# Kernel optimization log

Measured on AMD Instinct MI355X. Metric: run time of the kernel, lower is better.

The kernel has to match this reference:

```python
import jax, jax.numpy as jnp
import numpy as np

B, DX, DY, H, K = 16384, 128, 128, 2048, 16
MIN_BIN = 1e-3   # min bin width/height (nflows convention)
MIN_DERIV = 1e-3  # min knot derivative


def setup_inputs() -> dict:
    key = jax.random.key(0)
    k0, k1, k2, k3 = jax.random.split(key, 4)
    x = jax.random.normal(k0, (B, DX), jnp.float32)
    y = jax.random.uniform(k1, (B, DY), jnp.float32, minval=1e-4, maxval=1.0 - 1e-4)
    W1 = jax.random.normal(k2, (DX, H), jnp.float32) / np.sqrt(DX).astype(np.float32)
    b1 = jnp.zeros((H,), jnp.float32)
    W2 = jax.random.normal(k3, (H, DY * (3 * K + 1)), jnp.float32) / np.sqrt(H).astype(np.float32)
    b2 = jnp.zeros((DY * (3 * K + 1),), jnp.float32)
    return {"x": x, "y": y, "W1": W1, "b1": b1, "W2": W2, "b2": b2}


def _rq_spline(y, pdf):
    # y: [B, D] in (0,1); pdf: [B, D, 3K+1] unnormalized spline params
    w_un, h_un, d_un = pdf[..., :K], pdf[..., K:2 * K], pdf[..., 2 * K:]
    widths = MIN_BIN + (1.0 - K * MIN_BIN) * jax.nn.softmax(w_un, axis=-1)   # [B,D,K]
    heights = MIN_BIN + (1.0 - K * MIN_BIN) * jax.nn.softmax(h_un, axis=-1)  # [B,D,K]
    derivs = MIN_DERIV + jax.nn.softplus(d_un)                               # [B,D,K+1]

    pad = [(0, 0), (0, 0), (1, 0)]
    cw = jnp.pad(jnp.cumsum(widths, axis=-1), pad)    # knot x-positions [B,D,K+1]
    ch = jnp.pad(jnp.cumsum(heights, axis=-1), pad)   # knot y-positions [B,D,K+1]

    # data-dependent bin lookup (searchsorted equivalent, vectorized)
    idx = jnp.clip(jnp.sum(y[..., None] >= cw, axis=-1) - 1, 0, K - 1)  # [B,D]
    g = lambda a: jnp.take_along_axis(a, idx[..., None], axis=-1)[..., 0]
    xk, yk = g(cw), g(ch)
    wk, hk = g(widths), g(heights)
    dk = g(derivs)
    dk1 = jnp.take_along_axis(derivs, idx[..., None] + 1, axis=-1)[..., 0]

    s = hk / wk                      # bin slope
    t = (y - xk) / wk                # theta in [0,1]
    omt = 1.0 - t
    denom = s + (dk1 + dk - 2.0 * s) * t * omt
    out = yk + hk * (s * t * t + dk * t * omt) / denom
    deriv = s * s * (dk1 * t * t + 2.0 * s * t * omt + dk * omt * omt) / (denom * denom)
    dlogp = jnp.sum(jnp.log(deriv), axis=-1, keepdims=True)  # [B,1]
    return out, dlogp


def reference(x, y, W1, b1, W2, b2):
    # conditioner MLP: x -> spline params
    h = jax.nn.relu(x @ W1 + b1)
    pdf = (h @ W2 + b2).reshape(x.shape[0], DY, 3 * K + 1)
    return _rq_spline(y, pdf)
```

## Files before the change

### kernel.cpp

```cpp
#include <hip/hip_runtime.h>
#include <hip/hip_fp16.h>
#include <cstdint>
#include <cstddef>

#define B_ROWS 16384
#define DX 128
#define DYDIM 128
#define HDIM 2048
#define NPARAM 49
#define NCOL 6272
#define NPAD 6400

typedef __attribute__((ext_vector_type(8))) _Float16 half8v;
typedef __attribute__((ext_vector_type(4))) float f32x4;

__global__ void k_f32_to_f16(const float* __restrict__ in, _Float16* __restrict__ out, int n) {
  int i = blockIdx.x * 256 + threadIdx.x;
  if (i < n) out[i] = (_Float16)in[i];
}

__global__ void k_transpose_f16(const float* __restrict__ in, _Float16* __restrict__ out, int R, int C) {
  __shared__ float tile[32][33];
  int c0 = blockIdx.x * 32, r0 = blockIdx.y * 32;
  int tx = threadIdx.x;
  for (int i = threadIdx.y; i < 32; i += 8)
    tile[i][tx] = in[(size_t)(r0 + i) * C + c0 + tx];
  __syncthreads();
  for (int i = threadIdx.y; i < 32; i += 8)
    out[(size_t)(c0 + i) * R + r0 + tx] = (_Float16)tile[tx][i];
}

__global__ __launch_bounds__(256) void k_gemm1(
    const _Float16* __restrict__ A, const _Float16* __restrict__ Bt,
    const float* __restrict__ bias, _Float16* __restrict__ C,
    int M, int N, int K) {
  __shared__ _Float16 Abuf[128 * 32];
  __shared__ _Float16 Bbuf[128 * 32];
  const int t = threadIdx.x;
  const int l = t & 63;
  const int w = t >> 6;
  int bx = blockIdx.x, by = blockIdx.y;
  {
    const int nx = gridDim.x;
    const int nwg = nx * gridDim.y;
    const int lin = by * nx + bx;
    const int cpx = nwg >> 3;
    const int sw = (lin & 7) * cpx + (lin >> 3);
    bx = sw % nx;
    by = sw / nx;
  }
  const int tileM = by * 128;
  const int tileN = bx * 128;
  const int wm = w >> 1, wn = w & 1;
  const int srow = w * 16 + (l >> 2);
  const int skel = (l & 3) * 8;
  const char* Ag = (const char*)(A + (size_t)(tileM + srow) * K + skel);
  const char* Bg = (const char*)(Bt + (size_t)(tileN + srow) * K + skel);
  const size_t gRowStep = (size_t)64 * K * 2;
  auto ldsA = (__attribute__((address_space(3))) char*)Abuf;
  auto ldsB = (__attribute__((address_space(3))) char*)Bbuf;
  const int ldsBase = w * 1024;
  f32x4 acc[4][4];
#pragma unroll
  for (int i = 0; i < 4; ++i)
#pragma unroll
    for (int j = 0; j < 4; ++j) acc[i][j] = (f32x4){0.f, 0.f, 0.f, 0.f};
  const int nk = K >> 5;
#define STAGE1(kt)                                                                             \
  do {                                                                                         \
    size_t koff = (size_t)(kt) * 64;                                                           \
    __builtin_amdgcn_global_load_lds(                                                          \
        (const __attribute__((address_space(1))) uint32_t*)(Ag + koff),                        \
        (__attribute__((address_space(3))) uint32_t*)(ldsA + ldsBase), 16, 0, 0);              \
    __builtin_amdgcn_global_load_lds(                                                          \
        (const __attribute__((address_space(1))) uint32_t*)(Ag + koff + gRowStep),             \
        (__attribute__((address_space(3))) uint32_t*)(ldsA + 4096 + ldsBase), 16, 0, 0);       \
    __builtin_amdgcn_global_load_lds(                                                          \
        (const __attribute__((address_space(1))) uint32_t*)(Bg + koff),                        \
        (__attribute__((address_space(3))) uint32_t*)(ldsB + ldsBase), 16, 0, 0);              \
    __builtin_amdgcn_global_load_lds(                                                          \
        (const __attribute__((address_space(1))) uint32_t*)(Bg + koff + gRowStep),             \
        (__attribute__((address_space(3))) uint32_t*)(ldsB + 4096 + ldsBase), 16, 0, 0);       \
  } while (0)
  STAGE1(0);
  const int abase = (wm * 64 + (l & 15)) * 32 + (l >> 4) * 8;
  const int bbase = (wn * 64 + (l & 15)) * 32 + (l >> 4) * 8;
  for (int kt = 0; kt < nk; ++kt) {
    __syncthreads();
    half8v av[4], bv[4];
#pragma unroll
    for (int mf = 0; mf < 4; ++mf)
      av[mf] = *(const half8v*)((const _Float16*)Abuf + abase + mf * 512);
#pragma unroll
    for (int nf = 0; nf < 4; ++nf)
      bv[nf] = *(const half8v*)((const _Float16*)Bbuf + bbase + nf * 512);
#pragma unroll
    for (int mf = 0; mf < 4; ++mf)
#pragma unroll
      for (int nf = 0; nf < 4; ++nf)
        acc[mf][nf] = __builtin_amdgcn_mfma_f32_16x16x32_f16(av[mf], bv[nf], acc[mf][nf], 0, 0, 0);
    __syncthreads();
    if (kt + 1 < nk) STAGE1(kt + 1);
  }
#undef STAGE1
  const int crow0 = tileM + wm * 64 + (l >> 4) * 4;
  const int ccol0 = tileN + wn * 64 + (l & 15);
#pragma unroll
  for (int nf = 0; nf < 4; ++nf) {
    const int col = ccol0 + nf * 16;
    const float bvv = bias[col];
#pragma unroll
    for (int mf = 0; mf < 4; ++mf) {
#pragma unroll
      for (int j = 0; j < 4; ++j) {
        const int row = crow0 + mf * 16 + j;
        float v = fmaxf(acc[mf][nf][j] + bvv, 0.f);
        C[(size_t)row * N + col] = (_Float16)v;
      }
    }
  }
}

__global__ __launch_bounds__(512, 2) void k_gemm2(
    const _Float16* __restrict__ A, const _Float16* __restrict__ Bt,
    const float* __restrict__ bias, _Float16* __restrict__ C, int M) {
  constexpr int K = HDIM;
  constexpr int K2 = K * 2;
  constexpr int NT = K / 64;
  constexpr int ITERS = NT / 2;

  __shared__ char smem[131072];

  const int t = threadIdx.x;
  const int l = t & 63;
  const int w = t >> 6;
  const int wm = w >> 2;
  const int wn = w & 3;
  const int rlo = l & 15;
  const int khi = l >> 4;
  const int wOff = w * 1024;

  int bx = blockIdx.x, by = blockIdx.y;
  {
    const int nx = gridDim.x;
    const int nwg = nx * gridDim.y;
    const int lin = by * nx + bx;
    const int cpx = nwg >> 3;
    const int sw = (lin & 7) * cpx + (lin >> 3);
    bx = sw % nx;
    by = sw / nx;
  }
  const int tileM = by * 256;
  const int tileN = bx * 256;

  int rowj[2], kbj[2];
#pragma unroll
  for (int j = 0; j < 2; ++j) {
    const int phys = j * 8192 + t * 16;
    const int b = phys ^ (((phys >> 9) & 1) << 5);
    rowj[j] = ((b >> 11) << 4) + ((b >> 6) & 15);
    kbj[j] = (((b >> 10) & 1) << 6) + (b & 63);
  }
  const char* pA[2][2];
  const char* pB[2][2];
#pragma unroll
  for (int half = 0; half < 2; ++half)
#pragma unroll
    for (int j = 0; j < 2; ++j) {
      pA[half][j] = (const char*)A + (size_t)(tileM + half * 128 + rowj[j]) * K2 + kbj[j];
      pB[half][j] = (const char*)Bt + (size_t)(tileN + half * 128 + rowj[j]) * K2 + kbj[j];
    }

  auto lds3 = (__attribute__((address_space(3))) char*)smem;

#define LDSA(d, half) ((d) * 32768 + (half) * 16384)
#define LDSB(d, half) (65536 + (d) * 32768 + (half) * 16384)
#define GLDS(srcp, ldsoff)                                                                   \
  __builtin_amdgcn_global_load_lds(                                                           \
      (const __attribute__((address_space(1))) uint32_t*)(srcp),                              \
      (__attribute__((address_space(3))) uint32_t*)(lds3 + (ldsoff) + wOff), 16, 0, 0)
#define STG(op, d, half, kt)                                                                  \
  do {                                                                                        \
    GLDS(p##op[half][0] + (size_t)(kt) * 128, LDS##op(d, half));                              \
    GLDS(p##op[half][1] + (size_t)(kt) * 128, LDS##op(d, half) + 8192);                       \
  } while (0)
#define VM(n) asm volatile("s_waitcnt vmcnt(" #n ")" ::: "memory")
#define NOSTG ((void)0)
#define NOW ((void)0)
#define CFENCE asm volatile("" ::: "memory")

  const int swz = (rlo & 8) ? 32 : 0;
  const int lane16 = rlo * 64 + ((khi * 16) ^ swz);
  const int aW = wm * 8192 + lane16;
  const int bW = 65536 + wn * 4096 + lane16;

  half8v b000, b001, b010, b011, b100, b101, b110, b111;
  f32x4 acc[8][4];
#pragma unroll
  for (int i = 0; i < 8; ++i)
#pragma unroll
    for (int j = 0; j < 4; ++j) acc[i][j] = (f32x4){0.f, 0.f, 0.f, 0.f};

#define MF(fi, gj, av, bv) \
  acc[fi][gj] = __builtin_amdgcn_mfma_f32_16x16x32_f16(av, bv, acc[fi][gj], 0, 0, 0)

#define PHX(d, q, LOADB, WAITS, ...)                                                          \
  do {                                                                                        \
    const int aB = (d) * 32768 + ((q) >> 1) * 16384 + ((q) & 1) * 4096 + aW;                  \
    half8v a00 = *(const half8v*)(smem + aB);                                  \
    half8v a01 = *(const half8v*)(smem + aB + 1024);                           \
    half8v a10 = *(const half8v*)(smem + aB + 2048);                           \
    half8v a11 = *(const half8v*)(smem + aB + 3072);                           \
    if (LOADB) {                                                                              \
      const int bB = (d) * 32768 + bW;                                                        \
      b000 = *(const half8v*)(smem + bB);                                                     \
      b001 = *(const half8v*)(smem + bB + 1024);                                              \
      b010 = *(const half8v*)(smem + bB + 2048);                                              \
      b011 = *(const half8v*)(smem + bB + 3072);                                              \
      b100 = *(const half8v*)(smem + bB + 16384);                                             \
      b101 = *(const half8v*)(smem + bB + 17408);                                             \
      b110 = *(const half8v*)(smem + bB + 18432);                                             \
      b111 = *(const half8v*)(smem + bB + 19456);                                             \
    }                                                                                         \
    __VA_ARGS__;                                                                              \
    WAITS;                                                                                    \
    CFENCE;                                                                                   \
    __builtin_amdgcn_s_barrier();                                                             \
    asm volatile("s_waitcnt lgkmcnt(0)" ::: "memory");                                        \
    __builtin_amdgcn_s_setprio(1);                                                            \
    {                                                                                         \
      constexpr int f0 = ((q) >> 1) * 4 + ((q) & 1) * 2;                                      \
      MF(f0 + 0, 0, a00, b000); MF(f0 + 0, 0, a01, b001);                                     \
      MF(f0 + 0, 1, a00, b010); MF(f0 + 0, 1, a01, b011);                                     \
      MF(f0 + 0, 2, a00, b100); MF(f0 + 0, 2, a01, b101);                                     \
      MF(f0 + 0, 3, a00, b110); MF(f0 + 0, 3, a01, b111);                                     \
      MF(f0 + 1, 0, a10, b000); MF(f0 + 1, 0, a11, b001);                                     \
      MF(f0 + 1, 1, a10, b010); MF(f0 + 1, 1, a11, b011);                                     \
      MF(f0 + 1, 2, a10, b100); MF(f0 + 1, 2, a11, b101);                                     \
      MF(f0 + 1, 3, a10, b110); MF(f0 + 1, 3, a11, b111);                                     \
    }                                                                                         \
    __builtin_amdgcn_s_setprio(0);                                                            \
    CFENCE;                                                                                   \
    __builtin_amdgcn_s_barrier();                                                             \
  } while (0)

  STG(B, 0, 0, 0);
  STG(B, 0, 1, 0);
  STG(A, 0, 0, 0);
  STG(A, 0, 1, 0);
  STG(B, 1, 0, 1);
  STG(B, 1, 1, 1);
  STG(A, 1, 0, 1);
  VM(6);
  CFENCE;
  __builtin_amdgcn_s_barrier();

  for (int it = 0; it < ITERS - 1; ++it) {
    const int kt = 2 * it;
    PHX(0, 0, 1, NOW, STG(A, 1, 1, kt + 1));
    PHX(0, 1, 0, NOW, STG(B, 0, 0, kt + 2));
    PHX(0, 2, 0, NOW, STG(B, 0, 1, kt + 2); STG(A, 0, 0, kt + 2));
    PHX(0, 3, 0, VM(8), NOSTG);
    PHX(1, 0, 1, NOW, STG(A, 0, 1, kt + 2));
    PHX(1, 1, 0, VM(10), STG(B, 1, 0, kt + 3));
    PHX(1, 2, 0, NOW, STG(B, 1, 1, kt + 3); STG(A, 1, 0, kt + 3));
    PHX(1, 3, 0, VM(6), NOSTG);
  }
  PHX(0, 0, 1, NOW, STG(A, 1, 1, NT - 1));
  PHX(0, 1, 0, NOW, NOSTG);
  PHX(0, 2, 0, NOW, NOSTG);
  PHX(0, 3, 0, VM(2), NOSTG);
  PHX(1, 0, 1, NOW, NOSTG);
  PHX(1, 1, 0, VM(0), NOSTG);
  PHX(1, 2, 0, NOW, NOSTG);
  PHX(1, 3, 0, NOW, NOSTG);

#undef PHX
#undef MF
#undef STG
#undef GLDS
#undef LDSA
#undef LDSB

#pragma unroll
  for (int fi = 0; fi < 8; ++fi) {
    const int r0 = tileM + (((fi >> 2) * 2 + wm) << 6) + ((fi & 3) << 4) + khi * 4;
#pragma unroll
    for (int gj = 0; gj < 4; ++gj) {
      const int c = tileN + (((gj >> 1) * 4 + wn) << 5) + ((gj & 1) << 4) + rlo;
      if (c < NCOL) {
        const float bvv = bias[c];
#pragma unroll
        for (int j = 0; j < 4; ++j)
          C[(size_t)(r0 + j) * NCOL + c] = (_Float16)(acc[fi][gj][j] + bvv);
      }
    }
  }
}

__global__ __launch_bounds__(128) void k_spline(
    const _Float16* __restrict__ pdf,
    const float* __restrict__ y,
    float* __restrict__ out,
    float* __restrict__ dlogp) {
  alignas(16) __shared__ _Float16 row16[NCOL];
  __shared__ float red[128];
  const int b = blockIdx.x;
  const int d = threadIdx.x;
  const _Float16* p = pdf + (size_t)b * NCOL;
  for (int i = d; i < NCOL / 8; i += 128)
    ((half8v*)row16)[i] = ((const half8v*)p)[i];
  __syncthreads();
  const _Float16* q = &row16[d * NPARAM];

  float mw = -1e30f, mh = -1e30f;
#pragma unroll
  for (int j = 0; j < 16; ++j) {
    mw = fmaxf(mw, (float)q[j]);
    mh = fmaxf(mh, (float)q[16 + j]);
  }
  float sw = 0.f, sh = 0.f;
#pragma unroll
  for (int j = 0; j < 16; ++j) {
    sw += __expf((float)q[j] - mw);
    sh += __expf((float)q[16 + j] - mh);
  }
  const float rw = 0.984f / sw, rh = 0.984f / sh;
  const float yv = y[(size_t)b * DYDIM + d];

  float cws = 0.f, chs = 0.f, xk = 0.f, yk = 0.f, wk = 1.f, hk = 1.f;
  int idx = 0;
#pragma unroll
  for (int j = 0; j < 16; ++j) {
    float wj = 0.001f + rw * __expf((float)q[j] - mw);
    float hj = 0.001f + rh * __expf((float)q[16 + j] - mh);
    if (yv >= cws) { idx = j; xk = cws; yk = chs; wk = wj; hk = hj; }
    cws += wj;
    chs += hj;
  }
  const float du0 = (float)q[32 + idx], du1 = (float)q[33 + idx];
  const float dk  = 0.001f + fmaxf(du0, 0.f) + log1pf(__expf(-fabsf(du0)));
  const float dk1 = 0.001f + fmaxf(du1, 0.f) + log1pf(__expf(-fabsf(du1)));

  const float s = hk / wk;
  const float tt = (yv - xk) / wk;
  const float omt = 1.f - tt;
  const float dnm = s + (dk1 + dk - 2.f * s) * tt * omt;
  const float o = yk + hk * (s * tt * tt + dk * tt * omt) / dnm;
  const float dr = s * s * (dk1 * tt * tt + 2.f * s * tt * omt + dk * omt * omt) / (dnm * dnm);

  out[(size_t)b * DYDIM + d] = o;
  red[d] = __logf(dr);
  __syncthreads();
#pragma unroll
  for (int s2 = 64; s2 > 0; s2 >>= 1) {
    if (d < s2) red[d] += red[d + s2];
    __syncthreads();
  }
  if (d == 0) dlogp[b] = red[0];
}

extern "C" void kernel_launch(void* const* d_in, const int* in_sizes, int n_in,
                              void* d_out, int out_size, void* d_ws, size_t ws_size,
                              hipStream_t stream) {
  const float* x  = (const float*)d_in[0];
  const float* y  = (const float*)d_in[1];
  const float* W1 = (const float*)d_in[2];
  const float* b1 = (const float*)d_in[3];
  const float* W2 = (const float*)d_in[4];
  const float* b2 = (const float*)d_in[5];
  float* out = (float*)d_out;
  float* dlogp = out + (size_t)B_ROWS * DYDIM;

  char* ws = (char*)d_ws;
  _Float16* w2t = (_Float16*)ws;
  _Float16* h   = w2t + (size_t)NPAD * HDIM;
  _Float16* pdf = h + (size_t)B_ROWS * HDIM;
  _Float16* xb  = pdf;
  _Float16* w1t = xb + (size_t)B_ROWS * DX;

  const size_t fixed = ((size_t)NPAD * HDIM + (size_t)B_ROWS * HDIM) * 2;
  int crows = 8192;
  if (ws_size >= fixed + (size_t)16384 * NCOL * 2)       crows = 16384;
  else if (ws_size >= fixed + (size_t)14336 * NCOL * 2)  crows = 14336;
  else if (ws_size >= fixed + (size_t)12288 * NCOL * 2)  crows = 12288;

  k_f32_to_f16<<<(B_ROWS * DX + 255) / 256, 256, 0, stream>>>(x, xb, B_ROWS * DX);
  k_transpose_f16<<<dim3(HDIM / 32, DX / 32), dim3(32, 8), 0, stream>>>(W1, w1t, DX, HDIM);
  k_transpose_f16<<<dim3(NCOL / 32, HDIM / 32), dim3(32, 8), 0, stream>>>(W2, w2t, HDIM, NCOL);

  k_gemm1<<<dim3(HDIM / 128, B_ROWS / 128), 256, 0, stream>>>(
      xb, w1t, b1, h, B_ROWS, HDIM, DX);

  int done = 0;
  while (done < B_ROWS) {
    const int cr = (B_ROWS - done < crows) ? (B_ROWS - done) : crows;
    k_gemm2<<<dim3(NPAD / 256, cr / 256), 512, 0, stream>>>(
        h + (size_t)done * HDIM, w2t, b2, pdf, cr);
    k_spline<<<cr, 128, 0, stream>>>(pdf, y + (size_t)done * DYDIM,
                                     out + (size_t)done * DYDIM, dlogp + done);
    done += cr;
  }
}
```

Baseline: 545.0 us.

## Fuse spline evaluation into GEMM2 epilogue with dimension-aligned permuted W2 tiles

W2 is transposed into a permuted layout so that each 256-column N-tile holds whole 49-parameter groups (5 output dims, 245 columns). The GEMM2 epilogue writes the tile into swizzled LDS and evaluates the rational-quadratic spline there. This removes the fp16 pdf round trip through global memory and the separate spline kernel. Per-tile log-det partial sums go to a workspace buffer and a small reduction kernel adds them. The cost is extra padding work (26 tiles instead of 25, partly empty), a heavier epilogue, and removal of one LDS wait in the MFMA phase macro.

```diff
diff --git a/kernel.cpp b/kernel.cpp
--- a/kernel.cpp
+++ b/kernel.cpp
@@ -9,7 +9,8 @@
 #define HDIM 2048
 #define NPARAM 49
 #define NCOL 6272
-#define NPAD 6400
+#define NTILES 26
+#define W2PROWS (NTILES * 256)
 
 typedef __attribute__((ext_vector_type(8))) _Float16 half8v;
 typedef __attribute__((ext_vector_type(4))) float f32x4;
@@ -28,6 +29,21 @@
   __syncthreads();
   for (int i = threadIdx.y; i < 32; i += 8)
     out[(size_t)(c0 + i) * R + r0 + tx] = (_Float16)tile[tx][i];
+}
+
+__global__ void k_transpose_perm(const float* __restrict__ in, _Float16* __restrict__ out) {
+  __shared__ float tile[32][33];
+  int c0 = blockIdx.x * 32, r0 = blockIdx.y * 32;
+  int tx = threadIdx.x;
+  for (int i = threadIdx.y; i < 32; i += 8)
+    tile[i][tx] = in[(size_t)(r0 + i) * NCOL + c0 + tx];
+  __syncthreads();
+  for (int i = threadIdx.y; i < 32; i += 8) {
+    int g = c0 + i;
+    int t = g / 245;
+    int cc = g - t * 245;
+    out[(size_t)(t * 256 + cc) * HDIM + r0 + tx] = (_Float16)tile[tx][i];
+  }
 }
 
 __global__ __launch_bounds__(256) void k_gemm1(
@@ -121,15 +137,17 @@
   }
 }
 
-__global__ __launch_bounds__(512, 2) void k_gemm2(
+__global__ __launch_bounds__(512, 2) void k_gemm2s(
     const _Float16* __restrict__ A, const _Float16* __restrict__ Bt,
-    const float* __restrict__ bias, _Float16* __restrict__ C, int M) {
+    const float* __restrict__ bias, const float* __restrict__ y,
+    float* __restrict__ outp, float* __restrict__ gpart, int M) {
   constexpr int K = HDIM;
   constexpr int K2 = K * 2;
   constexpr int NT = K / 64;
   constexpr int ITERS = NT / 2;
 
   __shared__ char smem[131072];
+  __shared__ float red[512];
 
   const int t = threadIdx.x;
   const int l = t & 63;
@@ -207,10 +225,10 @@
 #define PHX(d, q, LOADB, WAITS, ...)                                                          \
   do {                                                                                        \
     const int aB = (d) * 32768 + ((q) >> 1) * 16384 + ((q) & 1) * 4096 + aW;                  \
-    half8v a00 = *(const half8v*)(smem + aB);                                  \
-    half8v a01 = *(const half8v*)(smem + aB + 1024);                           \
-    half8v a10 = *(const half8v*)(smem + aB + 2048);                           \
-    half8v a11 = *(const half8v*)(smem + aB + 3072);                           \
+    half8v a00 = *(const half8v*)(smem + aB);                                                 \
+    half8v a01 = *(const half8v*)(smem + aB + 1024);                                          \
+    half8v a10 = *(const half8v*)(smem + aB + 2048);                                          \
+    half8v a11 = *(const half8v*)(smem + aB + 3072);                                          \
     if (LOADB) {                                                                              \
       const int bB = (d) * 32768 + bW;                                                        \
       b000 = *(const half8v*)(smem + bB);                                                     \
@@ -226,7 +244,7 @@
     WAITS;                                                                                    \
     CFENCE;                                                                                   \
     __builtin_amdgcn_s_barrier();                                                             \
-    asm volatile("s_waitcnt lgkmcnt(0)" ::: "memory");                                        \
+    CFENCE;                                                                                   \
     __builtin_amdgcn_s_setprio(1);                                                            \
     {                                                                                         \
       constexpr int f0 = ((q) >> 1) * 4 + ((q) & 1) * 2;                                      \
@@ -282,82 +300,93 @@
 #undef LDSA
 #undef LDSB
 
+  const int RCt = (bx < 25) ? 245 : 147;
+  const int nd  = (bx < 25) ? 5 : 3;
+
 #pragma unroll
   for (int fi = 0; fi < 8; ++fi) {
-    const int r0 = tileM + (((fi >> 2) * 2 + wm) << 6) + ((fi & 3) << 4) + khi * 4;
+    const int r0l = (((fi >> 2) * 2 + wm) << 6) + ((fi & 3) << 4) + khi * 4;
 #pragma unroll
     for (int gj = 0; gj < 4; ++gj) {
-      const int c = tileN + (((gj >> 1) * 4 + wn) << 5) + ((gj & 1) << 4) + rlo;
-      if (c < NCOL) {
-        const float bvv = bias[c];
-#pragma unroll
-        for (int j = 0; j < 4; ++j)
-          C[(size_t)(r0 + j) * NCOL + c] = (_Float16)(acc[fi][gj][j] + bvv);
+      const int c = (((gj >> 1) * 4 + wn) << 5) + ((gj & 1) << 4) + rlo;
+      if (c < RCt) {
+        const float bvv = bias[245 * bx + c];
+#pragma unroll
+        for (int j = 0; j < 4; ++j) {
+          const int r = r0l + j;
+          *(_Float16*)(smem + r * 512 + ((2 * c) ^ ((r & 31) << 4))) =
+              (_Float16)(acc[fi][gj][j] + bvv);
+        }
       }
     }
   }
-}
-
-__global__ __launch_bounds__(128) void k_spline(
-    const _Float16* __restrict__ pdf,
-    const float* __restrict__ y,
-    float* __restrict__ out,
-    float* __restrict__ dlogp) {
-  alignas(16) __shared__ _Float16 row16[NCOL];
-  __shared__ float red[128];
-  const int b = blockIdx.x;
-  const int d = threadIdx.x;
-  const _Float16* p = pdf + (size_t)b * NCOL;
-  for (int i = d; i < NCOL / 8; i += 128)
-    ((half8v*)row16)[i] = ((const half8v*)p)[i];
   __syncthreads();
-  const _Float16* q = &row16[d * NPARAM];
-
-  float mw = -1e30f, mh = -1e30f;
-#pragma unroll
-  for (int j = 0; j < 16; ++j) {
-    mw = fmaxf(mw, (float)q[j]);
-    mh = fmaxf(mh, (float)q[16 + j]);
-  }
-  float sw = 0.f, sh = 0.f;
-#pragma unroll
-  for (int j = 0; j < 16; ++j) {
-    sw += __expf((float)q[j] - mw);
-    sh += __expf((float)q[16 + j] - mh);
-  }
-  const float rw = 0.984f / sw, rh = 0.984f / sh;
-  const float yv = y[(size_t)b * DYDIM + d];
-
-  float cws = 0.f, chs = 0.f, xk = 0.f, yk = 0.f, wk = 1.f, hk = 1.f;
-  int idx = 0;
-#pragma unroll
-  for (int j = 0; j < 16; ++j) {
-    float wj = 0.001f + rw * __expf((float)q[j] - mw);
-    float hj = 0.001f + rh * __expf((float)q[16 + j] - mh);
-    if (yv >= cws) { idx = j; xk = cws; yk = chs; wk = wj; hk = hj; }
-    cws += wj;
-    chs += hj;
-  }
-  const float du0 = (float)q[32 + idx], du1 = (float)q[33 + idx];
-  const float dk  = 0.001f + fmaxf(du0, 0.f) + log1pf(__expf(-fabsf(du0)));
-  const float dk1 = 0.001f + fmaxf(du1, 0.f) + log1pf(__expf(-fabsf(du1)));
-
-  const float s = hk / wk;
-  const float tt = (yv - xk) / wk;
-  const float omt = 1.f - tt;
-  const float dnm = s + (dk1 + dk - 2.f * s) * tt * omt;
-  const float o = yk + hk * (s * tt * tt + dk * tt * omt) / dnm;
-  const float dr = s * s * (dk1 * tt * tt + 2.f * s * tt * omt + dk * omt * omt) / (dnm * dnm);
-
-  out[(size_t)b * DYDIM + d] = o;
-  red[d] = __logf(dr);
+
+  float lsum = 0.f;
+#pragma unroll
+  for (int pass = 0; pass < 3; ++pass) {
+    const int task = pass * 512 + t;
+    const int d = task >> 8;
+    const int r = task & 255;
+    if (d < nd) {
+      const int rbase = r * 512;
+      const int rswz = (r & 31) << 4;
+      const int cb = 2 * (d * 49);
+#define LQ(j) ((float)*(const _Float16*)(smem + rbase + ((cb + 2 * (j)) ^ rswz)))
+      float mw = -1e30f, mh = -1e30f;
+#pragma unroll
+      for (int j = 0; j < 16; ++j) {
+        mw = fmaxf(mw, LQ(j));
+        mh = fmaxf(mh, LQ(16 + j));
+      }
+      float sw2 = 0.f, sh = 0.f;
+#pragma unroll
+      for (int j = 0; j < 16; ++j) {
+        sw2 += __expf(LQ(j) - mw);
+        sh += __expf(LQ(16 + j) - mh);
+      }
+      const float rw = 0.984f / sw2, rh = 0.984f / sh;
+      const int rg = tileM + r;
+      const int dg = 5 * bx + d;
+      const float yv = y[(size_t)rg * DYDIM + dg];
+
+      float cws = 0.f, chs = 0.f, xk = 0.f, yk = 0.f, wk = 1.f, hk = 1.f;
+      int idx = 0;
+#pragma unroll
+      for (int j = 0; j < 16; ++j) {
+        float wj = 0.001f + rw * __expf(LQ(j) - mw);
+        float hj = 0.001f + rh * __expf(LQ(16 + j) - mh);
+        if (yv >= cws) { idx = j; xk = cws; yk = chs; wk = wj; hk = hj; }
+        cws += wj;
+        chs += hj;
+      }
+      const float du0 = LQ(32 + idx), du1 = LQ(33 + idx);
+      const float dk  = 0.001f + fmaxf(du0, 0.f) + log1pf(__expf(-fabsf(du0)));
+      const float dk1 = 0.001f + fmaxf(du1, 0.f) + log1pf(__expf(-fabsf(du1)));
+
+      const float s = hk / wk;
+      const float tt = (yv - xk) / wk;
+      const float omt = 1.f - tt;
+      const float dnm = s + (dk1 + dk - 2.f * s) * tt * omt;
+      const float o = yk + hk * (s * tt * tt + dk * tt * omt) / dnm;
+      const float dr = s * s * (dk1 * tt * tt + 2.f * s * tt * omt + dk * omt * omt) / (dnm * dnm);
+
+      outp[(size_t)rg * DYDIM + dg] = o;
+      lsum += __logf(dr);
+#undef LQ
+    }
+  }
+  red[t] = lsum;
   __syncthreads();
-#pragma unroll
-  for (int s2 = 64; s2 > 0; s2 >>= 1) {
-    if (d < s2) red[d] += red[d + s2];
-    __syncthreads();
-  }
-  if (d == 0) dlogp[b] = red[0];
+  if (t < 256)
+    gpart[(size_t)bx * B_ROWS + (tileM + t)] = red[t] + red[t + 256];
+}
+
+__global__ void k_dlogp_reduce(const float* __restrict__ gpart, float* __restrict__ dlogp) {
+  int b = blockIdx.x * 256 + threadIdx.x;
+  float s = 0.f;
+  for (int tt = 0; tt < NTILES; ++tt) s += gpart[(size_t)tt * B_ROWS + b];
+  dlogp[b] = s;
 }
 
 extern "C" void kernel_launch(void* const* d_in, const int* in_sizes, int n_in,
@@ -373,32 +402,21 @@
   float* dlogp = out + (size_t)B_ROWS * DYDIM;
 
   char* ws = (char*)d_ws;
-  _Float16* w2t = (_Float16*)ws;
-  _Float16* h   = w2t + (size_t)NPAD * HDIM;
-  _Float16* pdf = h + (size_t)B_ROWS * HDIM;
-  _Float16* xb  = pdf;
+  _Float16* w2p = (_Float16*)ws;
+  _Float16* h   = w2p + (size_t)W2PROWS * HDIM;
+  _Float16* xb  = h + (size_t)B_ROWS * HDIM;
   _Float16* w1t = xb + (size_t)B_ROWS * DX;
-
-  const size_t fixed = ((size_t)NPAD * HDIM + (size_t)B_ROWS * HDIM) * 2;
-  int crows = 8192;
-  if (ws_size >= fixed + (size_t)16384 * NCOL * 2)       crows = 16384;
-  else if (ws_size >= fixed + (size_t)14336 * NCOL * 2)  crows = 14336;
-  else if (ws_size >= fixed + (size_t)12288 * NCOL * 2)  crows = 12288;
+  float* gpart  = (float*)(w1t + (size_t)HDIM * DX);
 
   k_f32_to_f16<<<(B_ROWS * DX + 255) / 256, 256, 0, stream>>>(x, xb, B_ROWS * DX);
   k_transpose_f16<<<dim3(HDIM / 32, DX / 32), dim3(32, 8), 0, stream>>>(W1, w1t, DX, HDIM);
-  k_transpose_f16<<<dim3(NCOL / 32, HDIM / 32), dim3(32, 8), 0, stream>>>(W2, w2t, HDIM, NCOL);
+  k_transpose_perm<<<dim3(NCOL / 32, HDIM / 32), dim3(32, 8), 0, stream>>>(W2, w2p);
 
   k_gemm1<<<dim3(HDIM / 128, B_ROWS / 128), 256, 0, stream>>>(
       xb, w1t, b1, h, B_ROWS, HDIM, DX);
 
-  int done = 0;
-  while (done < B_ROWS) {
-    const int cr = (B_ROWS - done < crows) ? (B_ROWS - done) : crows;
-    k_gemm2<<<dim3(NPAD / 256, cr / 256), 512, 0, stream>>>(
-        h + (size_t)done * HDIM, w2t, b2, pdf, cr);
-    k_spline<<<cr, 128, 0, stream>>>(pdf, y + (size_t)done * DYDIM,
-                                     out + (size_t)done * DYDIM, dlogp + done);
-    done += cr;
-  }
-}
+  k_gemm2s<<<dim3(NTILES, B_ROWS / 256), 512, 0, stream>>>(
+      h, w2p, b2, y, out, gpart, B_ROWS);
+
+  k_dlogp_reduce<<<B_ROWS / 256, 256, 0, stream>>>(gpart, dlogp);
+}
```

After: 502.7 us. -7.8%, faster.
